# Optimization experiments

Measured on AMD Instinct MI355X. Metric: run time of the kernel, lower is better.

The kernel has to match this reference:

```python
import jax, jax.numpy as jnp
import numpy as np

HIST_SIZE = 200
DIM = 64
HIDDEN = 32
NEG_INF = -2.0**32 + 1.0  # matches tf padding constant


def setup_inputs() -> dict:
    key = jax.random.key(0)
    k1, k2, k3, k4, k5 = jax.random.split(key, 5)
    B = 4096
    cand = jax.random.normal(k1, (B, DIM), dtype=jnp.float32)
    hist = jax.random.normal(k2, (B, HIST_SIZE, DIM), dtype=jnp.float32)
    hisLens = jax.random.randint(k3, (B,), 0, HIST_SIZE, dtype=jnp.int32)
    # Glorot-normal-ish params
    attW1 = jax.random.normal(k4, (4 * DIM, HIDDEN), dtype=jnp.float32) * (2.0 / (4 * DIM + HIDDEN)) ** 0.5
    attB1 = jnp.zeros((HIDDEN,), dtype=jnp.float32)
    attW2 = jax.random.normal(k5, (HIDDEN, 1), dtype=jnp.float32) * (2.0 / (HIDDEN + 1)) ** 0.5
    attB2 = jnp.zeros((1,), dtype=jnp.float32)
    return {"candidate_embedding": cand, "hist_embeddings": hist, "hisLens": hisLens,
            "attW1": attW1, "attB1": attB1, "attW2": attW2, "attB2": attB2}


def reference(candidate_embedding, hist_embeddings, hisLens, attW1, attB1, attW2, attB2):
    # candidate: [B, d] -> broadcast over hist steps [B, S, d]
    cand = candidate_embedding[:, None, :]
    # per-step feature concat: [cand, hist, cand*hist, cand-hist] -> [B, S, 4d]
    z3 = jnp.concatenate([
        jnp.broadcast_to(cand, hist_embeddings.shape),
        hist_embeddings,
        cand * hist_embeddings,
        cand - hist_embeddings,
    ], axis=-1)
    # tiny 2-layer MLP scorer -> [B, S]
    h = jax.nn.relu(jnp.einsum('bsf,fh->bsh', z3, attW1) + attB1)
    scores = (jnp.einsum('bsh,ho->bso', h, attW2) + attB2)[..., 0]
    # sequence mask then scale (same order as original), softmax over hist dim
    mask = jnp.arange(HIST_SIZE)[None, :] < hisLens[:, None]
    scores = jnp.where(mask, scores, NEG_INF) / (DIM ** 0.5)
    w = jax.nn.softmax(scores, axis=-1)  # [B, S]
    # weighted sum of history embeddings -> [B, d]
    return jnp.einsum('bs,bsd->bd', w, hist_embeddings)
```

## Files before the change

kernel.cpp:

```cpp
#include <hip/hip_runtime.h>
#include <math.h>

#define HS    200
#define DIMV  64
#define HID   32
#define NTH   256
#define NBPB  4

typedef __attribute__((ext_vector_type(8))) short short8;
typedef __attribute__((ext_vector_type(4))) float f32x4;
typedef __bf16 bf2_t __attribute__((ext_vector_type(2)));
typedef float  f2_t  __attribute__((ext_vector_type(2)));

__device__ __forceinline__ unsigned cvt2(float x, float y) {
    f2_t f = {x, y};
    bf2_t bv = __builtin_convertvector(f, bf2_t);
    union { bf2_t b; unsigned u; } un;
    un.b = bv;
    return un.u;
}

template<int CTRL>
__device__ __forceinline__ float dpp_add(float x) {
    int y = __builtin_amdgcn_update_dpp(0, __float_as_int(x), CTRL, 0xF, 0xF, true);
    return x + __int_as_float(y);
}
#define ROR1  0x121
#define ROR2  0x122
#define ROR4  0x124
#define ROR8  0x128
#define QXOR1 0xB1
#define QXOR2 0x4E
#define HMIRR 0x141
__device__ __forceinline__ float swz_xor16(float x) {
    return __int_as_float(__builtin_amdgcn_ds_swizzle(__float_as_int(x), 0x401F));
}
__device__ __forceinline__ float rfl(float x) {
    return __int_as_float(__builtin_amdgcn_readfirstlane(__float_as_int(x)));
}


__global__ __launch_bounds__(NTH, 4) void din_attn_kernel(
    const float* __restrict__ cand,
    const float* __restrict__ hist,
    const int*   __restrict__ lens,
    const float* __restrict__ W1,
    const float* __restrict__ B1,
    const float* __restrict__ W2,
    const float* __restrict__ B2,
    float* __restrict__ out)
{
    __shared__ __align__(16) unsigned short s_Mt[NBPB][HID * 64];
    __shared__ float s_c[NBPB][HID];

    const int tid  = threadIdx.x;
    const int lane = tid & 63, wid = tid >> 6;
    const int b0   = blockIdx.x * NBPB;

    {
        const int h = tid & 31, fg = tid >> 5;
        float wbd[8], wcc[8];
        #pragma unroll
        for (int ff = 0; ff < 8; ++ff) {
            int f = fg * 8 + ff;
            wbd[ff] = W1[(DIMV + f) * HID + h] - W1[(3 * DIMV + f) * HID + h];
            wcc[ff] = W1[(2 * DIMV + f) * HID + h];
        }
        #pragma unroll
        for (int k = 0; k < NBPB; ++k) {
            const float* cb = cand + (size_t)(b0 + k) * DIMV + fg * 8;
            float4 cA = *(const float4*)cb;
            float4 cB = *(const float4*)(cb + 4);
            float cf[8] = {cA.x, cA.y, cA.z, cA.w, cB.x, cB.y, cB.z, cB.w};
            float m[8];
            #pragma unroll
            for (int ff = 0; ff < 8; ++ff) m[ff] = fmaf(cf[ff], wcc[ff], wbd[ff]);
            uint4 mw = make_uint4(cvt2(m[0], m[1]), cvt2(m[2], m[3]),
                                  cvt2(m[4], m[5]), cvt2(m[6], m[7]));
            *(uint4*)&s_Mt[k][h * 64 + (fg ^ (h & 7)) * 8] = mw;
        }
        const int hc = tid >> 3, fgc = tid & 7;
        float wad[8];
        #pragma unroll
        for (int ff = 0; ff < 8; ++ff) {
            int f = fgc * 8 + ff;
            wad[ff] = W1[f * HID + hc] + W1[(3 * DIMV + f) * HID + hc];
        }
        float b1 = B1[hc];
        #pragma unroll
        for (int k = 0; k < NBPB; ++k) {
            const float* cb = cand + (size_t)(b0 + k) * DIMV + fgc * 8;
            float4 cA = *(const float4*)cb;
            float4 cB = *(const float4*)(cb + 4);
            float p = cA.x * wad[0] + cA.y * wad[1] + cA.z * wad[2] + cA.w * wad[3]
                    + cB.x * wad[4] + cB.y * wad[5] + cB.z * wad[6] + cB.w * wad[7];
            p = dpp_add<QXOR1>(p);
            p = dpp_add<QXOR2>(p);
            p = dpp_add<HMIRR>(p);
            if ((tid & 7) == 0) s_c[k][hc] = p + b1;
        }
    }
    __syncthreads();

    const int b    = b0 + wid;
    const int len  = lens[b];
    const bool uni = (len == 0);
    const int nrow = uni ? HS : len;
    const int nt   = (nrow + 15) >> 4;
    const int lc   = lane & 15, lg = lane >> 4;
    const float* hb = hist + (size_t)b * (HS * DIMV);

    short8 b00 = *(const short8*)&s_Mt[wid][lc * 64        + ((lg)     ^ (lc & 7)) * 8];
    short8 b01 = *(const short8*)&s_Mt[wid][lc * 64        + ((4 + lg) ^ (lc & 7)) * 8];
    short8 b10 = *(const short8*)&s_Mt[wid][(16 + lc) * 64 + ((lg)     ^ (lc & 7)) * 8];
    short8 b11 = *(const short8*)&s_Mt[wid][(16 + lc) * 64 + ((4 + lg) ^ (lc & 7)) * 8];
    const float c0  = s_c[wid][lc],        c1  = s_c[wid][16 + lc];
    const float w20 = W2[lc] * 0.125f,     w21 = W2[16 + lc] * 0.125f;

    float m_run = -3.0e38f, l_acc = 0.f;
    float o0[8] = {0.f, 0.f, 0.f, 0.f, 0.f, 0.f, 0.f, 0.f};
    float o1[8] = {0.f, 0.f, 0.f, 0.f, 0.f, 0.f, 0.f, 0.f};

    for (int rt = 0; rt < nt; ++rt) {
        int s = rt * 16 + lc;
        if (s > nrow - 1) s = nrow - 1;
        const float* ap = hb + s * 64 + lg * 8;
        float4 A00 = *(const float4*)ap;
        float4 A01 = *(const float4*)(ap + 4);
        float4 A10 = *(const float4*)(ap + 32);
        float4 A11 = *(const float4*)(ap + 36);
        union { uint4 u; short8 s8; } u0, u1;
        u0.u = make_uint4(cvt2(A00.x, A00.y), cvt2(A00.z, A00.w),
                          cvt2(A01.x, A01.y), cvt2(A01.z, A01.w));
        u1.u = make_uint4(cvt2(A10.x, A10.y), cvt2(A10.z, A10.w),
                          cvt2(A11.x, A11.y), cvt2(A11.z, A11.w));

        f32x4 acc0 = {c0, c0, c0, c0};
        acc0 = __builtin_amdgcn_mfma_f32_16x16x32_bf16(u0.s8, b00, acc0, 0, 0, 0);
        acc0 = __builtin_amdgcn_mfma_f32_16x16x32_bf16(u1.s8, b01, acc0, 0, 0, 0);
        f32x4 acc1 = {c1, c1, c1, c1};
        acc1 = __builtin_amdgcn_mfma_f32_16x16x32_bf16(u0.s8, b10, acc1, 0, 0, 0);
        acc1 = __builtin_amdgcn_mfma_f32_16x16x32_bf16(u1.s8, b11, acc1, 0, 0, 0);

        float p[4];
        #pragma unroll
        for (int r = 0; r < 4; ++r)
            p[r] = fmaxf(acc0[r], 0.f) * w20 + fmaxf(acc1[r], 0.f) * w21;
        #pragma unroll
        for (int r = 0; r < 4; ++r) {
            p[r] = dpp_add<ROR1>(p[r]);
            p[r] = dpp_add<ROR2>(p[r]);
            p[r] = dpp_add<ROR4>(p[r]);
            p[r] = dpp_add<ROR8>(p[r]);
        }
        #pragma unroll
        for (int r = 0; r < 4; ++r) {
            int row = rt * 16 + lg * 4 + r;
            p[r] = (row < nrow) ? (uni ? 0.f : p[r]) : -4.0e9f;
        }
        float tmax = fmaxf(fmaxf(p[0], p[1]), fmaxf(p[2], p[3]));
        tmax = fmaxf(tmax, swz_xor16(tmax));
        tmax = fmaxf(tmax, __shfl_xor(tmax, 32));
        tmax = rfl(tmax);
        if (tmax > m_run + 8.f) {
            float sf = __expf(m_run - tmax);
            #pragma unroll
            for (int j = 0; j < 8; ++j) { o0[j] *= sf; o1[j] *= sf; }
            l_acc *= sf;
            m_run = tmax;
        }
        float e[4];
        #pragma unroll
        for (int r = 0; r < 4; ++r) e[r] = __expf(p[r] - m_run);
        l_acc += (e[0] + e[1]) + (e[2] + e[3]);

        float t0 = (lc & 1) ? e[1] : e[0];
        float t1 = (lc & 1) ? e[3] : e[2];
        float es = (lc & 2) ? t1 : t0;
        int   src = (((lc & 3) | ((lc >> 2) << 4)) << 2);
        float wrow = __int_as_float(
            __builtin_amdgcn_ds_bpermute(src, __float_as_int(es)));

        o0[0] = fmaf(wrow, A00.x, o0[0]); o0[1] = fmaf(wrow, A00.y, o0[1]);
        o0[2] = fmaf(wrow, A00.z, o0[2]); o0[3] = fmaf(wrow, A00.w, o0[3]);
        o0[4] = fmaf(wrow, A01.x, o0[4]); o0[5] = fmaf(wrow, A01.y, o0[5]);
        o0[6] = fmaf(wrow, A01.z, o0[6]); o0[7] = fmaf(wrow, A01.w, o0[7]);
        o1[0] = fmaf(wrow, A10.x, o1[0]); o1[1] = fmaf(wrow, A10.y, o1[1]);
        o1[2] = fmaf(wrow, A10.z, o1[2]); o1[3] = fmaf(wrow, A10.w, o1[3]);
        o1[4] = fmaf(wrow, A11.x, o1[4]); o1[5] = fmaf(wrow, A11.y, o1[5]);
        o1[6] = fmaf(wrow, A11.z, o1[6]); o1[7] = fmaf(wrow, A11.w, o1[7]);
    }

    l_acc += swz_xor16(l_acc);
    l_acc += __shfl_xor(l_acc, 32);
    const float inv = 1.0f / l_acc;
    #pragma unroll
    for (int j = 0; j < 8; ++j) {
        float x = o0[j];
        x = dpp_add<ROR1>(x); x = dpp_add<ROR2>(x);
        x = dpp_add<ROR4>(x); x = dpp_add<ROR8>(x);
        o0[j] = x * inv;
        float y = o1[j];
        y = dpp_add<ROR1>(y); y = dpp_add<ROR2>(y);
        y = dpp_add<ROR4>(y); y = dpp_add<ROR8>(y);
        o1[j] = y * inv;
    }
    if (lc == 0) {
        float* op = out + (size_t)b * DIMV + lg * 8;
        *(float4*)op        = make_float4(o0[0], o0[1], o0[2], o0[3]);
        *(float4*)(op + 4)  = make_float4(o0[4], o0[5], o0[6], o0[7]);
        *(float4*)(op + 32) = make_float4(o1[0], o1[1], o1[2], o1[3]);
        *(float4*)(op + 36) = make_float4(o1[4], o1[5], o1[6], o1[7]);
    }
}

extern "C" void kernel_launch(void* const* d_in, const int* in_sizes, int n_in,
                              void* d_out, int out_size, void* d_ws, size_t ws_size,
                              hipStream_t stream) {
    const float* cand = (const float*)d_in[0];
    const float* hist = (const float*)d_in[1];
    const int*   lens = (const int*)d_in[2];
    const float* W1   = (const float*)d_in[3];
    const float* B1   = (const float*)d_in[4];
    const float* W2   = (const float*)d_in[5];
    const float* B2   = (const float*)d_in[6];
    float* out = (float*)d_out;

    const int B = in_sizes[0] / DIMV;
    const int GRID = B / NBPB;
    din_attn_kernel<<<GRID, NTH, 0, stream>>>(cand, hist, lens, W1, B1, W2, B2, out);
}
```

Baseline: 32.68 us.

## Split each batch row's history across two waves with a flash-style merge

Each block now handles two batch rows instead of four, with two waves per row. Each wave processes interleaved history steps (even or odd) and keeps its own running max, sum and weighted accumulator. A second LDS stage merges the two partial softmax states and writes the normalized output. The aim is to halve the serial per-wave loop length and double the grid, to better hide memory latency and balance uneven lengths. The cost is an extra block barrier, a small LDS combine step, and duplicated per-block prologue work because there are more blocks.

```diff
diff --git a/kernel.cpp b/kernel.cpp
--- a/kernel.cpp
+++ b/kernel.cpp
@@ -5,7 +5,7 @@
 #define DIMV  64
 #define HID   32
 #define NTH   256
-#define NBPB  4
+#define NB    2
 
 typedef __attribute__((ext_vector_type(8))) short short8;
 typedef __attribute__((ext_vector_type(4))) float f32x4;
@@ -50,12 +50,14 @@
     const float* __restrict__ B2,
     float* __restrict__ out)
 {
-    __shared__ __align__(16) unsigned short s_Mt[NBPB][HID * 64];
-    __shared__ float s_c[NBPB][HID];
+    __shared__ __align__(16) unsigned short s_Mt[NB][HID * 64];
+    __shared__ float s_c[NB][HID];
+    __shared__ __align__(16) float s_comb[4][DIMV];
+    __shared__ float s_m[4], s_l[4];
 
     const int tid  = threadIdx.x;
     const int lane = tid & 63, wid = tid >> 6;
-    const int b0   = blockIdx.x * NBPB;
+    const int b0   = blockIdx.x * NB;
 
     {
         const int h = tid & 31, fg = tid >> 5;
@@ -67,7 +69,7 @@
             wcc[ff] = W1[(2 * DIMV + f) * HID + h];
         }
         #pragma unroll
-        for (int k = 0; k < NBPB; ++k) {
+        for (int k = 0; k < NB; ++k) {
             const float* cb = cand + (size_t)(b0 + k) * DIMV + fg * 8;
             float4 cA = *(const float4*)cb;
             float4 cB = *(const float4*)(cb + 4);
@@ -88,7 +90,7 @@
         }
         float b1 = B1[hc];
         #pragma unroll
-        for (int k = 0; k < NBPB; ++k) {
+        for (int k = 0; k < NB; ++k) {
             const float* cb = cand + (size_t)(b0 + k) * DIMV + fgc * 8;
             float4 cA = *(const float4*)cb;
             float4 cB = *(const float4*)(cb + 4);
@@ -102,28 +104,31 @@
     }
     __syncthreads();
 
-    const int b    = b0 + wid;
+    const int kb   = wid >> 1, hf = wid & 1;
+    const int b    = b0 + kb;
     const int len  = lens[b];
     const bool uni = (len == 0);
-    const int nrow = uni ? HS : len;
-    const int nt   = (nrow + 15) >> 4;
-    const int lc   = lane & 15, lg = lane >> 4;
+    const int nrow  = uni ? HS : len;
+    const int nhalf = (nrow + 1 - hf) >> 1;
+    const int nt    = (nhalf + 15) >> 4;
+    const int lc    = lane & 15, lg = lane >> 4;
     const float* hb = hist + (size_t)b * (HS * DIMV);
 
-    short8 b00 = *(const short8*)&s_Mt[wid][lc * 64        + ((lg)     ^ (lc & 7)) * 8];
-    short8 b01 = *(const short8*)&s_Mt[wid][lc * 64        + ((4 + lg) ^ (lc & 7)) * 8];
-    short8 b10 = *(const short8*)&s_Mt[wid][(16 + lc) * 64 + ((lg)     ^ (lc & 7)) * 8];
-    short8 b11 = *(const short8*)&s_Mt[wid][(16 + lc) * 64 + ((4 + lg) ^ (lc & 7)) * 8];
-    const float c0  = s_c[wid][lc],        c1  = s_c[wid][16 + lc];
-    const float w20 = W2[lc] * 0.125f,     w21 = W2[16 + lc] * 0.125f;
+    short8 b00 = *(const short8*)&s_Mt[kb][lc * 64        + ((lg)     ^ (lc & 7)) * 8];
+    short8 b01 = *(const short8*)&s_Mt[kb][lc * 64        + ((4 + lg) ^ (lc & 7)) * 8];
+    short8 b10 = *(const short8*)&s_Mt[kb][(16 + lc) * 64 + ((lg)     ^ (lc & 7)) * 8];
+    short8 b11 = *(const short8*)&s_Mt[kb][(16 + lc) * 64 + ((4 + lg) ^ (lc & 7)) * 8];
+    const float c0  = s_c[kb][lc],     c1  = s_c[kb][16 + lc];
+    const float w20 = W2[lc] * 0.125f, w21 = W2[16 + lc] * 0.125f;
 
     float m_run = -3.0e38f, l_acc = 0.f;
     float o0[8] = {0.f, 0.f, 0.f, 0.f, 0.f, 0.f, 0.f, 0.f};
     float o1[8] = {0.f, 0.f, 0.f, 0.f, 0.f, 0.f, 0.f, 0.f};
 
     for (int rt = 0; rt < nt; ++rt) {
-        int s = rt * 16 + lc;
-        if (s > nrow - 1) s = nrow - 1;
+        int i = rt * 16 + lc;
+        if (i > nhalf - 1) i = nhalf - 1;
+        const int s = 2 * i + hf;
         const float* ap = hb + s * 64 + lg * 8;
         float4 A00 = *(const float4*)ap;
         float4 A01 = *(const float4*)(ap + 4);
@@ -156,7 +161,7 @@
         #pragma unroll
         for (int r = 0; r < 4; ++r) {
             int row = rt * 16 + lg * 4 + r;
-            p[r] = (row < nrow) ? (uni ? 0.f : p[r]) : -4.0e9f;
+            p[r] = (row < nhalf) ? (uni ? 0.f : p[r]) : -4.0e9f;
         }
         float tmax = fmaxf(fmaxf(p[0], p[1]), fmaxf(p[2], p[3]));
         tmax = fmaxf(tmax, swz_xor16(tmax));
@@ -193,24 +198,35 @@
 
     l_acc += swz_xor16(l_acc);
     l_acc += __shfl_xor(l_acc, 32);
-    const float inv = 1.0f / l_acc;
     #pragma unroll
     for (int j = 0; j < 8; ++j) {
         float x = o0[j];
         x = dpp_add<ROR1>(x); x = dpp_add<ROR2>(x);
         x = dpp_add<ROR4>(x); x = dpp_add<ROR8>(x);
-        o0[j] = x * inv;
+        o0[j] = x;
         float y = o1[j];
         y = dpp_add<ROR1>(y); y = dpp_add<ROR2>(y);
         y = dpp_add<ROR4>(y); y = dpp_add<ROR8>(y);
-        o1[j] = y * inv;
+        o1[j] = y;
     }
     if (lc == 0) {
-        float* op = out + (size_t)b * DIMV + lg * 8;
-        *(float4*)op        = make_float4(o0[0], o0[1], o0[2], o0[3]);
-        *(float4*)(op + 4)  = make_float4(o0[4], o0[5], o0[6], o0[7]);
-        *(float4*)(op + 32) = make_float4(o1[0], o1[1], o1[2], o1[3]);
-        *(float4*)(op + 36) = make_float4(o1[4], o1[5], o1[6], o1[7]);
+        float* d = &s_comb[wid][lg * 8];
+        *(float4*)d        = make_float4(o0[0], o0[1], o0[2], o0[3]);
+        *(float4*)(d + 4)  = make_float4(o0[4], o0[5], o0[6], o0[7]);
+        *(float4*)(d + 32) = make_float4(o1[0], o1[1], o1[2], o1[3]);
+        *(float4*)(d + 36) = make_float4(o1[4], o1[5], o1[6], o1[7]);
+        if (lane == 0) { s_m[wid] = m_run; s_l[wid] = l_acc; }
+    }
+    __syncthreads();
+
+    if (wid < NB) {
+        const int w0 = 2 * wid, w1 = 2 * wid + 1;
+        const float m0 = s_m[w0], m1 = s_m[w1];
+        const float M  = fmaxf(m0, m1);
+        const float a0 = __expf(m0 - M), a1 = __expf(m1 - M);
+        const float den = a0 * s_l[w0] + a1 * s_l[w1];
+        const float o   = a0 * s_comb[w0][lane] + a1 * s_comb[w1][lane];
+        out[(size_t)(b0 + wid) * DIMV + lane] = o / den;
     }
 }
 
@@ -227,6 +243,6 @@
     float* out = (float*)d_out;
 
     const int B = in_sizes[0] / DIMV;
-    const int GRID = B / NBPB;
+    const int GRID = B / NB;
     din_attn_kernel<<<GRID, NTH, 0, stream>>>(cand, hist, lens, W1, B1, W2, B2, out);
 }
```

Result: slower. 35.34 us (+8.1%).

## Double-buffer history row loads and reuse bf16 values for weighted sum

Applied to the files above, without the earlier changes.

Restructures the per-tile loop into a two-stage software pipeline: loads for tiles rt+2/rt+3 are issued before computing tile rt, so global memory latency overlaps with MFMA and softmax work. The weighted-sum accumulation now uses the bf16-converted values (unpacked by shift/mask) instead of the original fp32 registers, which frees the fp32 registers early. This reduces output precision to bf16 inputs for the weighted sum. Loads past the end are clamped to the last valid row, so the extra prefetches are redundant reads, not out-of-bounds accesses.

```diff
diff --git a/kernel.cpp b/kernel.cpp
--- a/kernel.cpp
+++ b/kernel.cpp
@@ -19,6 +19,8 @@
     un.b = bv;
     return un.u;
 }
+__device__ __forceinline__ float blo(unsigned u) { return __uint_as_float(u << 16); }
+__device__ __forceinline__ float bhi(unsigned u) { return __uint_as_float(u & 0xFFFF0000u); }
 
 template<int CTRL>
 __device__ __forceinline__ float dpp_add(float x) {
@@ -121,19 +123,22 @@
     float o0[8] = {0.f, 0.f, 0.f, 0.f, 0.f, 0.f, 0.f, 0.f};
     float o1[8] = {0.f, 0.f, 0.f, 0.f, 0.f, 0.f, 0.f, 0.f};
 
-    for (int rt = 0; rt < nt; ++rt) {
-        int s = rt * 16 + lc;
-        if (s > nrow - 1) s = nrow - 1;
-        const float* ap = hb + s * 64 + lg * 8;
-        float4 A00 = *(const float4*)ap;
-        float4 A01 = *(const float4*)(ap + 4);
-        float4 A10 = *(const float4*)(ap + 32);
-        float4 A11 = *(const float4*)(ap + 36);
+    auto ISSUE = [&](int rt, float4& X0, float4& X1, float4& X2, float4& X3) {
+        int i = rt * 16 + lc;
+        if (i > nrow - 1) i = nrow - 1;
+        const float* ap = hb + i * 64 + lg * 8;
+        X0 = *(const float4*)ap;
+        X1 = *(const float4*)(ap + 4);
+        X2 = *(const float4*)(ap + 32);
+        X3 = *(const float4*)(ap + 36);
+    };
+    auto COMP = [&](int rt, const float4& X0, const float4& X1,
+                            const float4& X2, const float4& X3) {
         union { uint4 u; short8 s8; } u0, u1;
-        u0.u = make_uint4(cvt2(A00.x, A00.y), cvt2(A00.z, A00.w),
-                          cvt2(A01.x, A01.y), cvt2(A01.z, A01.w));
-        u1.u = make_uint4(cvt2(A10.x, A10.y), cvt2(A10.z, A10.w),
-                          cvt2(A11.x, A11.y), cvt2(A11.z, A11.w));
+        u0.u = make_uint4(cvt2(X0.x, X0.y), cvt2(X0.z, X0.w),
+                          cvt2(X1.x, X1.y), cvt2(X1.z, X1.w));
+        u1.u = make_uint4(cvt2(X2.x, X2.y), cvt2(X2.z, X2.w),
+                          cvt2(X3.x, X3.y), cvt2(X3.z, X3.w));
 
         f32x4 acc0 = {c0, c0, c0, c0};
         acc0 = __builtin_amdgcn_mfma_f32_16x16x32_bf16(u0.s8, b00, acc0, 0, 0, 0);
@@ -181,14 +186,30 @@
         float wrow = __int_as_float(
             __builtin_amdgcn_ds_bpermute(src, __float_as_int(es)));
 
-        o0[0] = fmaf(wrow, A00.x, o0[0]); o0[1] = fmaf(wrow, A00.y, o0[1]);
-        o0[2] = fmaf(wrow, A00.z, o0[2]); o0[3] = fmaf(wrow, A00.w, o0[3]);
-        o0[4] = fmaf(wrow, A01.x, o0[4]); o0[5] = fmaf(wrow, A01.y, o0[5]);
-        o0[6] = fmaf(wrow, A01.z, o0[6]); o0[7] = fmaf(wrow, A01.w, o0[7]);
-        o1[0] = fmaf(wrow, A10.x, o1[0]); o1[1] = fmaf(wrow, A10.y, o1[1]);
-        o1[2] = fmaf(wrow, A10.z, o1[2]); o1[3] = fmaf(wrow, A10.w, o1[3]);
-        o1[4] = fmaf(wrow, A11.x, o1[4]); o1[5] = fmaf(wrow, A11.y, o1[5]);
-        o1[6] = fmaf(wrow, A11.z, o1[6]); o1[7] = fmaf(wrow, A11.w, o1[7]);
+        o0[0] = fmaf(wrow, blo(u0.u.x), o0[0]); o0[1] = fmaf(wrow, bhi(u0.u.x), o0[1]);
+        o0[2] = fmaf(wrow, blo(u0.u.y), o0[2]); o0[3] = fmaf(wrow, bhi(u0.u.y), o0[3]);
+        o0[4] = fmaf(wrow, blo(u0.u.z), o0[4]); o0[5] = fmaf(wrow, bhi(u0.u.z), o0[5]);
+        o0[6] = fmaf(wrow, blo(u0.u.w), o0[6]); o0[7] = fmaf(wrow, bhi(u0.u.w), o0[7]);
+        o1[0] = fmaf(wrow, blo(u1.u.x), o1[0]); o1[1] = fmaf(wrow, bhi(u1.u.x), o1[1]);
+        o1[2] = fmaf(wrow, blo(u1.u.y), o1[2]); o1[3] = fmaf(wrow, bhi(u1.u.y), o1[3]);
+        o1[4] = fmaf(wrow, blo(u1.u.z), o1[4]); o1[5] = fmaf(wrow, bhi(u1.u.z), o1[5]);
+        o1[6] = fmaf(wrow, blo(u1.u.w), o1[6]); o1[7] = fmaf(wrow, bhi(u1.u.w), o1[7]);
+    };
+
+    float4 F10, F11, F12, F13, F20, F21, F22, F23;
+    ISSUE(0, F10, F11, F12, F13);
+    ISSUE(1, F20, F21, F22, F23);
+    for (int rt = 0; rt < nt; rt += 2) {
+        {
+            float4 X0 = F10, X1 = F11, X2 = F12, X3 = F13;
+            ISSUE(rt + 2, F10, F11, F12, F13);
+            COMP(rt, X0, X1, X2, X3);
+        }
+        if (rt + 1 < nt) {
+            float4 X0 = F20, X1 = F21, X2 = F22, X3 = F23;
+            ISSUE(rt + 3, F20, F21, F22, F23);
+            COMP(rt + 1, X0, X1, X2, X3);
+        }
     }
 
     l_acc += swz_xor16(l_acc);
```

After: 32.81 us. No clear change (+0.4%).
